# Kernel tuning notes

Hardware: AMD Instinct MI355X
Metric: run time of the kernel (lower is better)

Reference implementation:

```python
import jax, jax.numpy as jnp
import numpy as np

TEMPERATURE = 1.0
NEG = -1e9
EPS = 1e-8


def setup_inputs() -> dict:
    key = jax.random.key(0)
    k1, k2, k3 = jax.random.split(key, 3)
    B, H = 524288, 32
    scores = jax.random.normal(k1, (B, H), dtype=jnp.float32)
    rankings = jax.random.randint(k2, (B, H), 0, 33, dtype=jnp.int32)
    mask = jax.random.randint(k3, (B, H), 0, 2, dtype=jnp.int32).astype(bool)
    return {"scores": scores, "rankings": rankings, "mask": mask}


def reference(scores, rankings, mask):
    B, H = scores.shape
    # effective validity: horse present AND has a ranking > 0 (top_k=None)
    m = mask & (rankings > 0)
    # masked, temperature-scaled scores; -1e9 entries underflow to exactly 0 in softmax
    s = jnp.where(m, scores / TEMPERATURE, NEG)
    p = jax.nn.softmax(s, axis=1)  # [B, H], ~0 at invalid slots

    n_valid = jnp.sum(m, axis=1)  # [B]
    # ideal order: valid horses sorted by ranking ascending (invalid pushed to end)
    rank_key = jnp.where(m, rankings, jnp.iinfo(jnp.int32).max)
    rank_order = jnp.argsort(rank_key, axis=1)          # stable sort
    # prediction order: valid horses in original index order (matches torch.where)
    pos_order = jnp.argsort(~m, axis=1)                 # stable: valid first

    q = jnp.take_along_axis(p, rank_order, axis=1)      # ideal_probs, aligned by list position
    pr = jnp.take_along_axis(p, pos_order, axis=1)      # pred_probs,  aligned by list position

    # positions >= n_valid are padding
    valid_pos = jnp.arange(H)[None, :] < n_valid[:, None]
    q_safe = jnp.where(valid_pos, q, 1.0)
    pr_safe = jnp.where(valid_pos, pr, 1.0)
    # KL(ideal || pred) with the original's log(pred + 1e-8)
    kl_terms = q_safe * (jnp.log(q_safe) - jnp.log(pr_safe + EPS))
    kl = jnp.sum(jnp.where(valid_pos, kl_terms, 0.0), axis=1)  # [B]

    # rows with <= 1 valid ranked horse are skipped entirely
    row_ok = n_valid > 1
    n_rows = jnp.maximum(jnp.sum(row_ok), 1)
    return jnp.sum(jnp.where(row_ok, kl, 0.0)) / n_rows  # reduction='mean'
```

## Files before the change

kernel.cpp:

```cpp
#include <hip/hip_runtime.h>
#include <stdint.h>


__global__ __launch_bounds__(256) void listwise_kernel(
    const float* __restrict__ scores,
    const int* __restrict__ rankings,
    const unsigned char* __restrict__ mask_u8,
    float* __restrict__ ws_kl,
    int* __restrict__ ws_cnt,
    int npairs)
{
    const int lane = threadIdx.x & 63;
    const int gl   = lane & 31;
    const int sh   = lane & 32;
    const uint32_t lmask = (1u << gl) - 1u;
    const int wid = threadIdx.x >> 6;
    const int wavesPerBlock = blockDim.x >> 6;
    const int gw = blockIdx.x * wavesPerBlock + wid;
    const int totWaves = gridDim.x * wavesPerBlock;

    unsigned char probe = mask_u8[lane];
    const bool mask_is_i32 =
        (__ballot(((lane & 3) != 0) && (probe != 0)) == 0ull);
    const int* mask_i32 = (const int*)mask_u8;

    float th_kl = 0.0f;
    int   th_cnt = 0;

    for (int pair = gw; pair < npairs; pair += totWaves) {
        const int base = pair * 64 + lane;
        const float s = scores[base];
        const int   r = rankings[base];
        const int   mk = mask_is_i32 ? mask_i32[base] : (int)mask_u8[base];
        const bool valid = (mk != 0) && (r > 0);

        const unsigned long long balv = __ballot(valid);
        const uint32_t vm = (uint32_t)(balv >> sh);
        const int nv = __popc(vm);

        float x = valid ? s : -3.0e38f;
        #pragma unroll
        for (int m = 16; m >= 1; m >>= 1) x = fmaxf(x, __shfl_xor(x, m));
        const float e = valid ? __expf(s - x) : 0.0f;
        float se = e;
        #pragma unroll
        for (int m = 16; m >= 1; m >>= 1) se += __shfl_xor(se, m);
        const float p = e / se;
        const float lp1 = __logf(p);
        const float lp2 = __logf(p + 1e-8f);

        const uint32_t v = ((uint32_t)(r - 1)) & 31u;
        uint32_t E = vm;
        int c_lt = 0;
        #pragma unroll
        for (int i = 4; i >= 0; --i) {
            const unsigned long long bb = __ballot((v >> i) & 1u);
            const uint32_t bi = (uint32_t)(bb >> sh);
            const uint32_t t = (v >> i) & 1u;
            c_lt += t ? __popc(E & ~bi) : 0;
            E &= t ? bi : ~bi;
        }
        const int eq_below = __popc(E & lmask);
        const int j_rank = c_lt + eq_below;
        const int j_pos  = __popc(vm & lmask);

        const int inv_pos = gl - j_pos;
        const int dst = valid ? j_pos : (nv + inv_pos);
        const int scat = __builtin_amdgcn_ds_permute((sh + dst) << 2,
                                                     __float_as_int(lp2));
        const int gidx = valid ? j_rank : 0;
        const float g = __int_as_float(
            __builtin_amdgcn_ds_bpermute((sh + gidx) << 2, scat));

        float term = valid ? p * (lp1 - g) : 0.0f;
        #pragma unroll
        for (int m = 16; m >= 1; m >>= 1) term += __shfl_xor(term, m);

        if (gl == 0 && nv > 1) { th_kl += term; th_cnt += 1; }
    }

    #pragma unroll
    for (int m = 32; m >= 1; m >>= 1) {
        th_kl  += __shfl_xor(th_kl, m);
        th_cnt += __shfl_xor(th_cnt, m);
    }
    __shared__ float s_kl[8];
    __shared__ int   s_cnt[8];
    if (lane == 0) { s_kl[wid] = th_kl; s_cnt[wid] = th_cnt; }
    __syncthreads();
    if (threadIdx.x == 0) {
        float k = 0.0f; int c = 0;
        for (int i = 0; i < wavesPerBlock; ++i) { k += s_kl[i]; c += s_cnt[i]; }
        atomicAdd(ws_kl, k);
        atomicAdd(ws_cnt, c);
    }
}

__global__ void finalize_kernel(const float* __restrict__ ws_kl,
                                const int* __restrict__ ws_cnt,
                                float* __restrict__ out)
{
    if (threadIdx.x == 0) {
        int c = *ws_cnt;
        if (c < 1) c = 1;
        out[0] = *ws_kl / (float)c;
    }
}

extern "C" void kernel_launch(void* const* d_in, const int* in_sizes, int n_in,
                              void* d_out, int out_size, void* d_ws, size_t ws_size,
                              hipStream_t stream) {
    const float* scores = (const float*)d_in[0];
    const int* rankings = (const int*)d_in[1];
    const unsigned char* mask = (const unsigned char*)d_in[2];
    float* out = (float*)d_out;

    const int total = in_sizes[0];
    const int npairs = total / 64;

    float* wsf = (float*)d_ws;
    int*   wsi = (int*)d_ws;

    hipMemsetAsync(d_ws, 0, 8, stream);

    const int threads = 256;
    const int blocks = 2048;
    listwise_kernel<<<blocks, threads, 0, stream>>>(
        scores, rankings, mask, wsf, wsi + 1, npairs);

    finalize_kernel<<<1, 64, 0, stream>>>(wsf, wsi + 1, out);
}
```

Measured before the change: 237.8 us.

## Simplify per-row KL algebraically and use ds_swizzle row reductions

The per-row KL is rewritten as sum(e_i*(s_i - s_perm(i)))/sum(e_i), so the log-softmax normaliser cancels. This removes the max reduction, both logf calls and the per-element division, and the data permuted between lanes is now the raw score instead of a log-probability. The 32-lane sums use ds_swizzle instead of shuffle-xor. In exchange the max subtraction and the 1e-8 epsilon are dropped. That risks expf overflow for large scores and small numerical differences from the reference, though both are likely benign for normally distributed inputs.

```diff
diff --git a/kernel.cpp b/kernel.cpp
--- a/kernel.cpp
+++ b/kernel.cpp
@@ -1,6 +1,17 @@
 #include <hip/hip_runtime.h>
 #include <stdint.h>
 
+
+#define SWZ(x, pat) __int_as_float(__builtin_amdgcn_ds_swizzle(__float_as_int(x), pat))
+
+__device__ __forceinline__ float rowsum32(float x) {
+    x += SWZ(x, 0x041F);
+    x += SWZ(x, 0x081F);
+    x += SWZ(x, 0x101F);
+    x += SWZ(x, 0x201F);
+    x += SWZ(x, 0x401F);
+    return x;
+}
 
 __global__ __launch_bounds__(256) void listwise_kernel(
     const float* __restrict__ scores,
@@ -13,6 +24,7 @@
     const int lane = threadIdx.x & 63;
     const int gl   = lane & 31;
     const int sh   = lane & 32;
+    const bool hi_half = (sh != 0);
     const uint32_t lmask = (1u << gl) - 1u;
     const int wid = threadIdx.x >> 6;
     const int wavesPerBlock = blockDim.x >> 6;
@@ -35,48 +47,40 @@
         const bool valid = (mk != 0) && (r > 0);
 
         const unsigned long long balv = __ballot(valid);
-        const uint32_t vm = (uint32_t)(balv >> sh);
+        const uint32_t vm = hi_half ? (uint32_t)(balv >> 32) : (uint32_t)balv;
         const int nv = __popc(vm);
 
-        float x = valid ? s : -3.0e38f;
-        #pragma unroll
-        for (int m = 16; m >= 1; m >>= 1) x = fmaxf(x, __shfl_xor(x, m));
-        const float e = valid ? __expf(s - x) : 0.0f;
-        float se = e;
-        #pragma unroll
-        for (int m = 16; m >= 1; m >>= 1) se += __shfl_xor(se, m);
-        const float p = e / se;
-        const float lp1 = __logf(p);
-        const float lp2 = __logf(p + 1e-8f);
+        const float e = valid ? __expf(s) : 0.0f;
+        const float se = rowsum32(e);
 
         const uint32_t v = ((uint32_t)(r - 1)) & 31u;
         uint32_t E = vm;
         int c_lt = 0;
         #pragma unroll
         for (int i = 4; i >= 0; --i) {
-            const unsigned long long bb = __ballot((v >> i) & 1u);
-            const uint32_t bi = (uint32_t)(bb >> sh);
             const uint32_t t = (v >> i) & 1u;
+            const unsigned long long bb = __ballot(t != 0u);
+            const uint32_t bi = hi_half ? (uint32_t)(bb >> 32) : (uint32_t)bb;
             c_lt += t ? __popc(E & ~bi) : 0;
             E &= t ? bi : ~bi;
         }
-        const int eq_below = __popc(E & lmask);
-        const int j_rank = c_lt + eq_below;
+        const int j_rank = c_lt + __popc(E & lmask);
         const int j_pos  = __popc(vm & lmask);
 
-        const int inv_pos = gl - j_pos;
-        const int dst = valid ? j_pos : (nv + inv_pos);
+        const int dst = valid ? j_pos : (nv + (gl - j_pos));
         const int scat = __builtin_amdgcn_ds_permute((sh + dst) << 2,
-                                                     __float_as_int(lp2));
+                                                     __float_as_int(s));
         const int gidx = valid ? j_rank : 0;
         const float g = __int_as_float(
             __builtin_amdgcn_ds_bpermute((sh + gidx) << 2, scat));
 
-        float term = valid ? p * (lp1 - g) : 0.0f;
-        #pragma unroll
-        for (int m = 16; m >= 1; m >>= 1) term += __shfl_xor(term, m);
+        const float t1 = e * (s - g);
+        const float num = rowsum32(t1);
 
-        if (gl == 0 && nv > 1) { th_kl += term; th_cnt += 1; }
+        if (gl == 0 && nv > 1) {
+            th_kl += __fdividef(num, se);
+            th_cnt += 1;
+        }
     }
 
     #pragma unroll
```

Result: no change. 240.6 us (+1.2%).
